# Kernel tuning notes

Measured on AMD Instinct MI355X. Metric: run time of the kernel, lower is better.

Reference implementation:

```python
import jax, jax.numpy as jnp
import numpy as np

FS = 11        # filter_size
N_ITER = 5     # mean-field iterations


def _unfold(x, fs):
    """x: (B, C, Hp, Wp) padded -> patches (B, C, H, W, fs, fs) with
    patches[b,c,h,w,i,j] == x[b,c,h+i,w+j]."""
    B, C, Hp, Wp = x.shape
    H, W = Hp - fs + 1, Wp - fs + 1
    p = jax.lax.conv_general_dilated_patches(
        x.reshape(B * C, 1, Hp, Wp), (fs, fs), (1, 1), 'VALID')  # (B*C, fs*fs, H, W)
    return p.reshape(B, C, fs, fs, H, W).transpose(0, 1, 4, 5, 2, 3)


def _smoothing_filter(fs, inv_bw, spacings):
    """Gaussian spatial filter with zeroed center, shape (B, fs, fs)."""
    r = jnp.arange(-(fs // 2), fs // 2 + 1, dtype=spacings.dtype)
    d = jnp.stack(jnp.meshgrid(r, r, indexing='ij'))           # (2, fs, fs)
    d = d[None] * spacings[:, :, None, None]                   # (B, 2, fs, fs)
    f = jnp.exp(-jnp.sum((d * inv_bw) ** 2 / 2, axis=1))       # (B, fs, fs)
    return f.at[:, fs // 2, fs // 2].set(0.0)


def setup_inputs() -> dict:
    key = jax.random.key(0)
    k1, k2 = jax.random.split(key)
    B, C, CH, H, W = 2, 6, 3, 192, 192
    return {
        'x': jax.random.normal(k1, (B, C, H, W), dtype=jnp.float32),
        'features': jax.random.normal(k2, (B, CH, H, W), dtype=jnp.float32),
        'spatial_spacings': jnp.ones((B, 2), dtype=jnp.float32),
        'smoothing_weight': jnp.array(1.0, dtype=jnp.float32),
        'appearance_weight': jnp.array(1.0, dtype=jnp.float32),
        'inverse_smoothing_bandwidth': jnp.array(1.0, dtype=jnp.float32),
        'inverse_appearance_bandwidth': jnp.array(1.0, dtype=jnp.float32),
    }


def reference(x, features, spatial_spacings, smoothing_weight, appearance_weight,
              inverse_smoothing_bandwidth, inverse_appearance_bandwidth):
    fs, pad = FS, FS // 2
    B, C, H, W = x.shape
    pad_cfg = [(0, 0), (0, 0), (pad, pad), (pad, pad)]

    # Spatial Gaussian filter (iteration-independent).
    sf = _smoothing_filter(fs, inverse_smoothing_bandwidth, spatial_spacings)  # (B,fs,fs)

    # Bilateral (appearance) filter, also iteration-independent -> hoisted.
    fpatch = _unfold(jnp.pad(features, pad_cfg), fs)           # (B,ch,H,W,fs,fs)
    diffs = features[..., None, None] - fpatch
    af = jnp.exp(-jnp.sum((diffs * inverse_appearance_bandwidth) ** 2 / 2, axis=1))  # (B,H,W,fs,fs)
    af = af.at[..., fs // 2, fs // 2].set(0.0)

    # combined message filter: w_s * sf + w_a * sf * af  (center tap already zero)
    sfb = sf[:, None, None]                                    # (B,1,1,fs,fs)
    total_filter = smoothing_weight * jnp.broadcast_to(sfb, af.shape) + appearance_weight * sfb * af

    compat = -jnp.eye(C, dtype=x.dtype)                        # Potts compatibility mu(l,l') = -[l==l']
    negative_unary = x
    for _ in range(N_ITER):
        q = jax.nn.softmax(x, axis=1)
        qpatch = _unfold(jnp.pad(q, pad_cfg), fs)              # (B,C,H,W,fs,fs)
        msg = jnp.einsum('bhwij,bchwij->bchw', total_filter, qpatch)
        x = negative_unary - jnp.einsum('bjhw,jk->bkhw', msg, compat)
    return jax.nn.log_softmax(x, axis=1)
```

## Files before the change

### kernel.cpp

```cpp
#include <hip/hip_runtime.h>

#define HH 192
#define WW 192
#define BB 2
#define NC 6
#define FSZ 11
#define PAD 5
#define TW 96
#define TH 3
#define SWD 107
#define SHT 14
#define LA 107
#define HW (HH*WW)
#define BT 768

__device__ __forceinline__ unsigned pkbf(float a, float b) {
    unsigned ua = (__float_as_uint(a) + 0x8000u) >> 16;
    unsigned ub = (__float_as_uint(b) + 0x8000u) & 0xffff0000u;
    return ua | ub;
}
__device__ __forceinline__ float lo16(unsigned u){ return __uint_as_float(u << 16); }
__device__ __forceinline__ float hi16(unsigned u){ return __uint_as_float(u & 0xffff0000u); }

template<bool FIRST, bool LAST>
__global__ __launch_bounds__(BT, 3)
void crf_it(const float* __restrict__ xpl, const uint4* __restrict__ Ain,
            const float* __restrict__ f2in, const float* __restrict__ feats,
            const float* __restrict__ spac, const float* __restrict__ swp,
            const float* __restrict__ awp, const float* __restrict__ isbp,
            const float* __restrict__ iabp,
            uint4* __restrict__ Aout, float* __restrict__ f2out,
            float* __restrict__ outp)
{
    __shared__ uint4 A[SHT][LA];
    __shared__ float F2[SHT][LA];
    __shared__ float sfw[FSZ*FSZ];
    __shared__ float sfa[FSZ*FSZ];

    const int tid = threadIdx.x;
    const int b  = blockIdx.z;
    const int w0 = blockIdx.x * TW;
    const int h0 = blockIdx.y * TH;

    const float sw  = swp[0], aw = awp[0], isb = isbp[0], iab = iabp[0];
    const float s0  = spac[b*2], s1 = spac[b*2+1];
    const float sfac = iab * 0.70710678f;

    if (tid < FSZ*FSZ) {
        const int fi = tid / FSZ, fj = tid - (tid/FSZ)*FSZ;
        const float ri = (float)(fi-PAD) * s0 * isb;
        const float rj = (float)(fj-PAD) * s1 * isb;
        float sf = __expf(-0.5f*(ri*ri + rj*rj));
        if (fi == PAD && fj == PAD) sf = 0.f;
        sfw[tid] = sf * sw;
        sfa[tid] = sf * aw;
    }

    for (int idx = tid; idx < SHT*SWD; idx += BT) {
        const int sr = idx / SWD, sc = idx - (idx/SWD)*SWD;
        const int gh = h0 + sr - PAD, gw = w0 + sc - PAD;
        uint4 av = make_uint4(0u,0u,0u,0u);
        float f2v = 0.f;
        if (gh >= 0 && gh < HH && gw >= 0 && gw < WW) {
            if (FIRST) {
                const int off = gh*WW + gw;
                const float* xb = xpl + (size_t)b*NC*HW + off;
                const float v0 = xb[0], v1 = xb[HW], v2 = xb[2*HW];
                const float v3 = xb[3*HW], v4 = xb[4*HW], v5 = xb[5*HW];
                float m = fmaxf(fmaxf(fmaxf(v0,v1),fmaxf(v2,v3)),fmaxf(v4,v5));
                float q0=__expf(v0-m), q1=__expf(v1-m), q2=__expf(v2-m);
                float q3=__expf(v3-m), q4=__expf(v4-m), q5=__expf(v5-m);
                const float rs = 1.0f/(q0+q1+q2+q3+q4+q5);
                const float* fb = feats + (size_t)b*3*HW + off;
                const float g0 = fb[0]*sfac, g1 = fb[HW]*sfac;
                f2v = fb[2*HW]*sfac;
                av = make_uint4(pkbf(q0*rs,q1*rs), pkbf(q2*rs,q3*rs),
                                pkbf(q4*rs,q5*rs), pkbf(g0,g1));
            } else {
                const size_t p = (size_t)(b*HH + gh)*WW + gw;
                av  = Ain[p];
                f2v = f2in[p];
            }
        }
        A[sr][sc]  = av;
        F2[sr][sc] = f2v;
    }
    __syncthreads();

    const int w    = tid >> 6;
    const int l    = tid & 63;
    const int t3   = l >> 3;
    const int rb   = (l >> 1) & 3;
    const int hf   = l & 1;
    const int prow = w >> 2;
    const int cb   = (w & 3)*24 + t3*3;
    const int jb   = hf*6;
    const int jcnt = hf ? 5 : 6;

    float cf0[3], cf1[3], cf2[3];
    #pragma unroll
    for (int k = 0; k < 3; ++k) {
        const uint4 cav = A[prow+PAD][cb+k+PAD];
        cf0[k] = lo16(cav.w);
        cf1[k] = hi16(cav.w);
        cf2[k] = F2[prow+PAD][cb+k+PAD];
    }

    float ms[3][NC];
    #pragma unroll
    for (int k = 0; k < 3; ++k)
        #pragma unroll
        for (int c = 0; c < NC; ++c) ms[k][c] = 0.f;

    #pragma unroll
    for (int m = 0; m < 3; ++m) {
        const int i = rb + 4*m;
        const bool vrow = (i < FSZ);
        float srwR[6], sraR[6];
        #pragma unroll
        for (int d = 0; d < 6; ++d) {
            const bool v = vrow && (d < jcnt);
            srwR[d] = v ? sfw[i*FSZ + jb + d] : 0.f;
            sraR[d] = v ? sfa[i*FSZ + jb + d] : 0.f;
        }
        const uint4* Ar = &A[prow + i][cb + jb];
        const float* Fr = &F2[prow + i][cb + jb];
        #pragma unroll
        for (int a = 0; a < 8; ++a) {
            const uint4 av = Ar[a];
            const float g2 = Fr[a];
            const float q0 = lo16(av.x), q1 = hi16(av.x);
            const float q2 = lo16(av.y), q3 = hi16(av.y);
            const float q4 = lo16(av.z), q5 = hi16(av.z);
            const float g0 = lo16(av.w), g1 = hi16(av.w);
            #pragma unroll
            for (int k = 0; k < 3; ++k) {
                const int d = a - k;
                if (0 <= d && d < 6) {
                    const float d0 = cf0[k]-g0, d1 = cf1[k]-g1, d2 = cf2[k]-g2;
                    const float t  = fmaf(d2,d2, fmaf(d1,d1, d0*d0));
                    const float af = __expf(-t);
                    const float tf = fmaf(af, sraR[d], srwR[d]);
                    ms[k][0] = fmaf(tf,q0,ms[k][0]);
                    ms[k][1] = fmaf(tf,q1,ms[k][1]);
                    ms[k][2] = fmaf(tf,q2,ms[k][2]);
                    ms[k][3] = fmaf(tf,q3,ms[k][3]);
                    ms[k][4] = fmaf(tf,q4,ms[k][4]);
                    ms[k][5] = fmaf(tf,q5,ms[k][5]);
                }
            }
        }
    }

    #pragma unroll
    for (int k = 0; k < 3; ++k)
        #pragma unroll
        for (int c = 0; c < NC; ++c) {
            float v = ms[k][c];
            v += __shfl_xor(v, 1);
            v += __shfl_xor(v, 2);
            v += __shfl_xor(v, 4);
            ms[k][c] = v;
        }

    if ((l & 7) == 0) {
        #pragma unroll
        for (int k = 0; k < 3; ++k) {
            const int oh = h0 + prow, ow = w0 + cb + k;
            const size_t pb = (size_t)b*NC*HW + (size_t)oh*WW + ow;
            float xn[NC];
            #pragma unroll
            for (int c = 0; c < NC; ++c) xn[c] = ms[k][c] + xpl[pb + (size_t)c*HW];

            float m = xn[0];
            #pragma unroll
            for (int c = 1; c < NC; ++c) m = fmaxf(m, xn[c]);

            if (LAST) {
                float s = 0.f;
                #pragma unroll
                for (int c = 0; c < NC; ++c) s += __expf(xn[c]-m);
                const float lg = m + __logf(s);
                #pragma unroll
                for (int c = 0; c < NC; ++c) outp[pb + (size_t)c*HW] = xn[c] - lg;
            } else {
                float e[NC], s = 0.f;
                #pragma unroll
                for (int c = 0; c < NC; ++c) { e[c] = __expf(xn[c]-m); s += e[c]; }
                const float rs = 1.0f / s;
                const size_t p = (size_t)(b*HH + oh)*WW + ow;
                Aout[p] = make_uint4(pkbf(e[0]*rs,e[1]*rs), pkbf(e[2]*rs,e[3]*rs),
                                     pkbf(e[4]*rs,e[5]*rs), pkbf(cf0[k],cf1[k]));
                if (FIRST) f2out[p] = cf2[k];
            }
        }
    }
}

extern "C" void kernel_launch(void* const* d_in, const int* in_sizes, int n_in,
                              void* d_out, int out_size, void* d_ws, size_t ws_size,
                              hipStream_t stream)
{
    const float* x    = (const float*)d_in[0];
    const float* fts  = (const float*)d_in[1];
    const float* spc  = (const float*)d_in[2];
    const float* swp  = (const float*)d_in[3];
    const float* awp  = (const float*)d_in[4];
    const float* isbp = (const float*)d_in[5];
    const float* iabp = (const float*)d_in[6];
    float* out = (float*)d_out;

    uint4* A0  = (uint4*)d_ws;
    uint4* A1  = A0 + (size_t)BB*HW;
    float* f2s = (float*)(A1 + (size_t)BB*HW);

    dim3 grid(WW/TW, HH/TH, BB);
    dim3 blk(BT);

    crf_it<true ,false><<<grid, blk, 0, stream>>>(x, A1, f2s, fts, spc, swp, awp, isbp, iabp, A0, f2s, out);
    crf_it<false,false><<<grid, blk, 0, stream>>>(x, A0, f2s, fts, spc, swp, awp, isbp, iabp, A1, f2s, out);
    crf_it<false,false><<<grid, blk, 0, stream>>>(x, A1, f2s, fts, spc, swp, awp, isbp, iabp, A0, f2s, out);
    crf_it<false,false><<<grid, blk, 0, stream>>>(x, A0, f2s, fts, spc, swp, awp, isbp, iabp, A1, f2s, out);
    crf_it<false,true ><<<grid, blk, 0, stream>>>(x, A1, f2s, fts, spc, swp, awp, isbp, iabp, A0, f2s, out);
}
```

Measured before the change: 65.69 us.

## Fuse pairs of mean-field iterations per kernel with halo recomputation

Replaces the five per-iteration launches with two fused kernels, each doing two mean-field iterations, plus a final kernel for the last iteration and the log-softmax. Each fused block loads a double-width halo, recomputes the intermediate softmax for its padded region in shared memory, then applies the second filter pass. Tiles change to 24x12, and the last stage splits the filter rows across two threads per pixel. This cuts launches and the global round trips of the intermediate state, but adds a lot of redundant halo compute (the first stage covers a 22x34 region for a 12x24 output tile) in an exp-heavy, compute-bound loop.

```diff
diff --git a/kernel.cpp b/kernel.cpp
--- a/kernel.cpp
+++ b/kernel.cpp
@@ -6,13 +6,19 @@
 #define NC 6
 #define FSZ 11
 #define PAD 5
-#define TW 96
-#define TH 3
-#define SWD 107
-#define SHT 14
-#define LA 107
+#define TW 24
+#define TH 12
 #define HW (HH*WW)
-#define BT 768
+
+#define S1R 32
+#define S1C 45
+#define Q1R 22
+#define Q1C 34
+#define BTA 768
+
+#define S3R 22
+#define S3C 35
+#define BTB 576
 
 __device__ __forceinline__ unsigned pkbf(float a, float b) {
     unsigned ua = (__float_as_uint(a) + 0x8000u) >> 16;
@@ -22,51 +28,56 @@
 __device__ __forceinline__ float lo16(unsigned u){ return __uint_as_float(u << 16); }
 __device__ __forceinline__ float hi16(unsigned u){ return __uint_as_float(u & 0xffff0000u); }
 
-template<bool FIRST, bool LAST>
-__global__ __launch_bounds__(BT, 3)
-void crf_it(const float* __restrict__ xpl, const uint4* __restrict__ Ain,
-            const float* __restrict__ f2in, const float* __restrict__ feats,
-            const float* __restrict__ spac, const float* __restrict__ swp,
-            const float* __restrict__ awp, const float* __restrict__ isbp,
-            const float* __restrict__ iabp,
-            uint4* __restrict__ Aout, float* __restrict__ f2out,
-            float* __restrict__ outp)
+__device__ __forceinline__ void build_sf(int tid, float s0, float s1, float isb,
+                                         float swv, float awv, float* sfw, float* sfa)
 {
-    __shared__ uint4 A[SHT][LA];
-    __shared__ float F2[SHT][LA];
-    __shared__ float sfw[FSZ*FSZ];
-    __shared__ float sfa[FSZ*FSZ];
+    if (tid < FSZ*FSZ) {
+        const int fi = tid / FSZ, fj = tid - (tid/FSZ)*FSZ;
+        const float ri = (float)(fi-PAD)*s0*isb;
+        const float rj = (float)(fj-PAD)*s1*isb;
+        float sf = __expf(-0.5f*(ri*ri+rj*rj));
+        if (fi==PAD && fj==PAD) sf = 0.f;
+        sfw[tid] = sf*swv;
+        sfa[tid] = sf*awv;
+    }
+}
+
+template<bool FIRST>
+__global__ __launch_bounds__(BTA, 3)
+void crf_duo(const float* __restrict__ xpl, const uint4* __restrict__ Ain,
+             const float* __restrict__ f2in, const float* __restrict__ feats,
+             const float* __restrict__ spac, const float* __restrict__ swp,
+             const float* __restrict__ awp, const float* __restrict__ isbp,
+             const float* __restrict__ iabp,
+             uint4* __restrict__ Aout, float* __restrict__ f2out)
+{
+    __shared__ uint4 A1[S1R][S1C];
+    __shared__ float F2a[S1R][S1C];
+    __shared__ uint4 Q1[Q1R][Q1C];
+    __shared__ float sfw[FSZ*FSZ], sfa[FSZ*FSZ];
 
     const int tid = threadIdx.x;
     const int b  = blockIdx.z;
     const int w0 = blockIdx.x * TW;
     const int h0 = blockIdx.y * TH;
 
-    const float sw  = swp[0], aw = awp[0], isb = isbp[0], iab = iabp[0];
-    const float s0  = spac[b*2], s1 = spac[b*2+1];
+    const float sw = swp[0], aw = awp[0], isb = isbp[0], iab = iabp[0];
+    const float s0 = spac[b*2], s1 = spac[b*2+1];
     const float sfac = iab * 0.70710678f;
 
-    if (tid < FSZ*FSZ) {
-        const int fi = tid / FSZ, fj = tid - (tid/FSZ)*FSZ;
-        const float ri = (float)(fi-PAD) * s0 * isb;
-        const float rj = (float)(fj-PAD) * s1 * isb;
-        float sf = __expf(-0.5f*(ri*ri + rj*rj));
-        if (fi == PAD && fj == PAD) sf = 0.f;
-        sfw[tid] = sf * sw;
-        sfa[tid] = sf * aw;
-    }
-
-    for (int idx = tid; idx < SHT*SWD; idx += BT) {
-        const int sr = idx / SWD, sc = idx - (idx/SWD)*SWD;
-        const int gh = h0 + sr - PAD, gw = w0 + sc - PAD;
+    build_sf(tid, s0, s1, isb, sw, aw, sfw, sfa);
+
+    for (int idx = tid; idx < S1R*S1C; idx += BTA) {
+        const int sr = idx / S1C, sc = idx - (idx/S1C)*S1C;
+        const int gh = h0 - 2*PAD + sr, gw = w0 - 2*PAD + sc;
         uint4 av = make_uint4(0u,0u,0u,0u);
         float f2v = 0.f;
         if (gh >= 0 && gh < HH && gw >= 0 && gw < WW) {
             if (FIRST) {
                 const int off = gh*WW + gw;
                 const float* xb = xpl + (size_t)b*NC*HW + off;
-                const float v0 = xb[0], v1 = xb[HW], v2 = xb[2*HW];
-                const float v3 = xb[3*HW], v4 = xb[4*HW], v5 = xb[5*HW];
+                const float v0=xb[0], v1=xb[HW], v2=xb[2*HW];
+                const float v3=xb[3*HW], v4=xb[4*HW], v5=xb[5*HW];
                 float m = fmaxf(fmaxf(fmaxf(v0,v1),fmaxf(v2,v3)),fmaxf(v4,v5));
                 float q0=__expf(v0-m), q1=__expf(v1-m), q2=__expf(v2-m);
                 float q3=__expf(v3-m), q4=__expf(v4-m), q5=__expf(v5-m);
@@ -82,117 +93,199 @@
                 f2v = f2in[p];
             }
         }
+        A1[sr][sc]  = av;
+        F2a[sr][sc] = f2v;
+    }
+    __syncthreads();
+
+    if (tid < Q1R*Q1C) {
+        const int pr = tid / Q1C, pc = tid - (tid/Q1C)*Q1C;
+        const int gh = h0 - PAD + pr, gw = w0 - PAD + pc;
+        uint4 qv = make_uint4(0u,0u,0u,0u);
+        if (gh >= 0 && gh < HH && gw >= 0 && gw < WW) {
+            const unsigned cw = A1[pr+PAD][pc+PAD].w;
+            const float cf0 = lo16(cw), cf1 = hi16(cw);
+            const float cf2 = F2a[pr+PAD][pc+PAD];
+            float msg[NC];
+            #pragma unroll
+            for (int c = 0; c < NC; ++c) msg[c] = 0.f;
+            #pragma unroll 1
+            for (int i = 0; i < FSZ; ++i) {
+                const float* srw = &sfw[i*FSZ];
+                const float* sra = &sfa[i*FSZ];
+                #pragma unroll
+                for (int j = 0; j < FSZ; ++j) {
+                    const uint4 av = A1[pr+i][pc+j];
+                    const float g2 = F2a[pr+i][pc+j];
+                    const float g0 = lo16(av.w), g1 = hi16(av.w);
+                    const float d0 = cf0-g0, d1 = cf1-g1, d2 = cf2-g2;
+                    const float t  = fmaf(d2,d2, fmaf(d1,d1, d0*d0));
+                    const float tf = fmaf(__expf(-t), sra[j], srw[j]);
+                    msg[0] = fmaf(tf, lo16(av.x), msg[0]);
+                    msg[1] = fmaf(tf, hi16(av.x), msg[1]);
+                    msg[2] = fmaf(tf, lo16(av.y), msg[2]);
+                    msg[3] = fmaf(tf, hi16(av.y), msg[3]);
+                    msg[4] = fmaf(tf, lo16(av.z), msg[4]);
+                    msg[5] = fmaf(tf, hi16(av.z), msg[5]);
+                }
+            }
+            const float* up = xpl + (size_t)b*NC*HW + (size_t)gh*WW + gw;
+            float xn[NC];
+            #pragma unroll
+            for (int c = 0; c < NC; ++c) xn[c] = msg[c] + up[(size_t)c*HW];
+            float m = xn[0];
+            #pragma unroll
+            for (int c = 1; c < NC; ++c) m = fmaxf(m, xn[c]);
+            float e[NC], s = 0.f;
+            #pragma unroll
+            for (int c = 0; c < NC; ++c) { e[c] = __expf(xn[c]-m); s += e[c]; }
+            const float rs = 1.0f / s;
+            qv = make_uint4(pkbf(e[0]*rs,e[1]*rs), pkbf(e[2]*rs,e[3]*rs),
+                            pkbf(e[4]*rs,e[5]*rs), 0u);
+        }
+        Q1[tid / Q1C][tid - (tid/Q1C)*Q1C] = qv;
+    }
+    __syncthreads();
+
+    if (tid < 2*TH*TW) {
+        const int p = tid >> 1, h = tid & 1;
+        const int qr = p / TW, qc = p - (p/TW)*TW;
+        const unsigned cw = A1[qr+2*PAD][qc+2*PAD].w;
+        const float cf0 = lo16(cw), cf1 = hi16(cw);
+        const float cf2 = F2a[qr+2*PAD][qc+2*PAD];
+        float msg[NC];
+        #pragma unroll
+        for (int c = 0; c < NC; ++c) msg[c] = 0.f;
+        const int i0 = h ? 6 : 0, i1 = h ? FSZ : 6;
+        #pragma unroll 1
+        for (int i = i0; i < i1; ++i) {
+            const float* srw = &sfw[i*FSZ];
+            const float* sra = &sfa[i*FSZ];
+            #pragma unroll
+            for (int j = 0; j < FSZ; ++j) {
+                const uint4 qv = Q1[qr+i][qc+j];
+                const uint4 fv = A1[qr+i+PAD][qc+j+PAD];
+                const float g2 = F2a[qr+i+PAD][qc+j+PAD];
+                const float g0 = lo16(fv.w), g1 = hi16(fv.w);
+                const float d0 = cf0-g0, d1 = cf1-g1, d2 = cf2-g2;
+                const float t  = fmaf(d2,d2, fmaf(d1,d1, d0*d0));
+                const float tf = fmaf(__expf(-t), sra[j], srw[j]);
+                msg[0] = fmaf(tf, lo16(qv.x), msg[0]);
+                msg[1] = fmaf(tf, hi16(qv.x), msg[1]);
+                msg[2] = fmaf(tf, lo16(qv.y), msg[2]);
+                msg[3] = fmaf(tf, hi16(qv.y), msg[3]);
+                msg[4] = fmaf(tf, lo16(qv.z), msg[4]);
+                msg[5] = fmaf(tf, hi16(qv.z), msg[5]);
+            }
+        }
+        #pragma unroll
+        for (int c = 0; c < NC; ++c) msg[c] += __shfl_xor(msg[c], 1);
+
+        if (h == 0) {
+            const int oh = h0 + qr, ow = w0 + qc;
+            const size_t pb = (size_t)b*NC*HW + (size_t)oh*WW + ow;
+            float xn[NC];
+            #pragma unroll
+            for (int c = 0; c < NC; ++c) xn[c] = msg[c] + xpl[pb + (size_t)c*HW];
+            float m = xn[0];
+            #pragma unroll
+            for (int c = 1; c < NC; ++c) m = fmaxf(m, xn[c]);
+            float e[NC], s = 0.f;
+            #pragma unroll
+            for (int c = 0; c < NC; ++c) { e[c] = __expf(xn[c]-m); s += e[c]; }
+            const float rs = 1.0f / s;
+            const size_t op = (size_t)(b*HH + oh)*WW + ow;
+            Aout[op] = make_uint4(pkbf(e[0]*rs,e[1]*rs), pkbf(e[2]*rs,e[3]*rs),
+                                  pkbf(e[4]*rs,e[5]*rs), cw);
+            if (FIRST) f2out[op] = cf2;
+        }
+    }
+}
+
+__global__ __launch_bounds__(BTB, 2)
+void crf_fin(const float* __restrict__ xpl, const uint4* __restrict__ Ain,
+             const float* __restrict__ f2in,
+             const float* __restrict__ spac, const float* __restrict__ swp,
+             const float* __restrict__ awp, const float* __restrict__ isbp,
+             const float* __restrict__ iabp, float* __restrict__ outp)
+{
+    __shared__ uint4 A[S3R][S3C];
+    __shared__ float F2[S3R][S3C];
+    __shared__ float sfw[FSZ*FSZ], sfa[FSZ*FSZ];
+
+    const int tid = threadIdx.x;
+    const int b  = blockIdx.z;
+    const int w0 = blockIdx.x * TW;
+    const int h0 = blockIdx.y * TH;
+
+    const float sw = swp[0], aw = awp[0], isb = isbp[0];
+    const float s0 = spac[b*2], s1 = spac[b*2+1];
+
+    build_sf(tid, s0, s1, isb, sw, aw, sfw, sfa);
+
+    for (int idx = tid; idx < S3R*S3C; idx += BTB) {
+        const int sr = idx / S3C, sc = idx - (idx/S3C)*S3C;
+        const int gh = h0 - PAD + sr, gw = w0 - PAD + sc;
+        uint4 av = make_uint4(0u,0u,0u,0u);
+        float f2v = 0.f;
+        if (gh >= 0 && gh < HH && gw >= 0 && gw < WW) {
+            const size_t p = (size_t)(b*HH + gh)*WW + gw;
+            av  = Ain[p];
+            f2v = f2in[p];
+        }
         A[sr][sc]  = av;
         F2[sr][sc] = f2v;
     }
     __syncthreads();
 
-    const int w    = tid >> 6;
-    const int l    = tid & 63;
-    const int t3   = l >> 3;
-    const int rb   = (l >> 1) & 3;
-    const int hf   = l & 1;
-    const int prow = w >> 2;
-    const int cb   = (w & 3)*24 + t3*3;
-    const int jb   = hf*6;
-    const int jcnt = hf ? 5 : 6;
-
-    float cf0[3], cf1[3], cf2[3];
-    #pragma unroll
-    for (int k = 0; k < 3; ++k) {
-        const uint4 cav = A[prow+PAD][cb+k+PAD];
-        cf0[k] = lo16(cav.w);
-        cf1[k] = hi16(cav.w);
-        cf2[k] = F2[prow+PAD][cb+k+PAD];
-    }
-
-    float ms[3][NC];
-    #pragma unroll
-    for (int k = 0; k < 3; ++k)
+    if (tid < 2*TH*TW) {
+        const int p = tid >> 1, h = tid & 1;
+        const int qr = p / TW, qc = p - (p/TW)*TW;
+        const unsigned cw = A[qr+PAD][qc+PAD].w;
+        const float cf0 = lo16(cw), cf1 = hi16(cw);
+        const float cf2 = F2[qr+PAD][qc+PAD];
+        float msg[NC];
         #pragma unroll
-        for (int c = 0; c < NC; ++c) ms[k][c] = 0.f;
-
-    #pragma unroll
-    for (int m = 0; m < 3; ++m) {
-        const int i = rb + 4*m;
-        const bool vrow = (i < FSZ);
-        float srwR[6], sraR[6];
+        for (int c = 0; c < NC; ++c) msg[c] = 0.f;
+        const int i0 = h ? 6 : 0, i1 = h ? FSZ : 6;
+        #pragma unroll 1
+        for (int i = i0; i < i1; ++i) {
+            const float* srw = &sfw[i*FSZ];
+            const float* sra = &sfa[i*FSZ];
+            #pragma unroll
+            for (int j = 0; j < FSZ; ++j) {
+                const uint4 qv = A[qr+i][qc+j];
+                const float g2 = F2[qr+i][qc+j];
+                const float g0 = lo16(qv.w), g1 = hi16(qv.w);
+                const float d0 = cf0-g0, d1 = cf1-g1, d2 = cf2-g2;
+                const float t  = fmaf(d2,d2, fmaf(d1,d1, d0*d0));
+                const float tf = fmaf(__expf(-t), sra[j], srw[j]);
+                msg[0] = fmaf(tf, lo16(qv.x), msg[0]);
+                msg[1] = fmaf(tf, hi16(qv.x), msg[1]);
+                msg[2] = fmaf(tf, lo16(qv.y), msg[2]);
+                msg[3] = fmaf(tf, hi16(qv.y), msg[3]);
+                msg[4] = fmaf(tf, lo16(qv.z), msg[4]);
+                msg[5] = fmaf(tf, hi16(qv.z), msg[5]);
+            }
+        }
         #pragma unroll
-        for (int d = 0; d < 6; ++d) {
-            const bool v = vrow && (d < jcnt);
-            srwR[d] = v ? sfw[i*FSZ + jb + d] : 0.f;
-            sraR[d] = v ? sfa[i*FSZ + jb + d] : 0.f;
-        }
-        const uint4* Ar = &A[prow + i][cb + jb];
-        const float* Fr = &F2[prow + i][cb + jb];
-        #pragma unroll
-        for (int a = 0; a < 8; ++a) {
-            const uint4 av = Ar[a];
-            const float g2 = Fr[a];
-            const float q0 = lo16(av.x), q1 = hi16(av.x);
-            const float q2 = lo16(av.y), q3 = hi16(av.y);
-            const float q4 = lo16(av.z), q5 = hi16(av.z);
-            const float g0 = lo16(av.w), g1 = hi16(av.w);
-            #pragma unroll
-            for (int k = 0; k < 3; ++k) {
-                const int d = a - k;
-                if (0 <= d && d < 6) {
-                    const float d0 = cf0[k]-g0, d1 = cf1[k]-g1, d2 = cf2[k]-g2;
-                    const float t  = fmaf(d2,d2, fmaf(d1,d1, d0*d0));
-                    const float af = __expf(-t);
-                    const float tf = fmaf(af, sraR[d], srwR[d]);
-                    ms[k][0] = fmaf(tf,q0,ms[k][0]);
-                    ms[k][1] = fmaf(tf,q1,ms[k][1]);
-                    ms[k][2] = fmaf(tf,q2,ms[k][2]);
-                    ms[k][3] = fmaf(tf,q3,ms[k][3]);
-                    ms[k][4] = fmaf(tf,q4,ms[k][4]);
-                    ms[k][5] = fmaf(tf,q5,ms[k][5]);
-                }
-            }
-        }
-    }
-
-    #pragma unroll
-    for (int k = 0; k < 3; ++k)
-        #pragma unroll
-        for (int c = 0; c < NC; ++c) {
-            float v = ms[k][c];
-            v += __shfl_xor(v, 1);
-            v += __shfl_xor(v, 2);
-            v += __shfl_xor(v, 4);
-            ms[k][c] = v;
-        }
-
-    if ((l & 7) == 0) {
-        #pragma unroll
-        for (int k = 0; k < 3; ++k) {
-            const int oh = h0 + prow, ow = w0 + cb + k;
+        for (int c = 0; c < NC; ++c) msg[c] += __shfl_xor(msg[c], 1);
+
+        if (h == 0) {
+            const int oh = h0 + qr, ow = w0 + qc;
             const size_t pb = (size_t)b*NC*HW + (size_t)oh*WW + ow;
             float xn[NC];
             #pragma unroll
-            for (int c = 0; c < NC; ++c) xn[c] = ms[k][c] + xpl[pb + (size_t)c*HW];
-
+            for (int c = 0; c < NC; ++c) xn[c] = msg[c] + xpl[pb + (size_t)c*HW];
             float m = xn[0];
             #pragma unroll
             for (int c = 1; c < NC; ++c) m = fmaxf(m, xn[c]);
-
-            if (LAST) {
-                float s = 0.f;
-                #pragma unroll
-                for (int c = 0; c < NC; ++c) s += __expf(xn[c]-m);
-                const float lg = m + __logf(s);
-                #pragma unroll
-                for (int c = 0; c < NC; ++c) outp[pb + (size_t)c*HW] = xn[c] - lg;
-            } else {
-                float e[NC], s = 0.f;
-                #pragma unroll
-                for (int c = 0; c < NC; ++c) { e[c] = __expf(xn[c]-m); s += e[c]; }
-                const float rs = 1.0f / s;
-                const size_t p = (size_t)(b*HH + oh)*WW + ow;
-                Aout[p] = make_uint4(pkbf(e[0]*rs,e[1]*rs), pkbf(e[2]*rs,e[3]*rs),
-                                     pkbf(e[4]*rs,e[5]*rs), pkbf(cf0[k],cf1[k]));
-                if (FIRST) f2out[p] = cf2[k];
-            }
+            float s = 0.f;
+            #pragma unroll
+            for (int c = 0; c < NC; ++c) s += __expf(xn[c]-m);
+            const float lg = m + __logf(s);
+            #pragma unroll
+            for (int c = 0; c < NC; ++c) outp[pb + (size_t)c*HW] = xn[c] - lg;
         }
     }
 }
@@ -210,16 +303,13 @@
     const float* iabp = (const float*)d_in[6];
     float* out = (float*)d_out;
 
-    uint4* A0  = (uint4*)d_ws;
-    uint4* A1  = A0 + (size_t)BB*HW;
-    float* f2s = (float*)(A1 + (size_t)BB*HW);
+    uint4* S0  = (uint4*)d_ws;
+    uint4* S1  = S0 + (size_t)BB*HW;
+    float* f2s = (float*)(S1 + (size_t)BB*HW);
 
     dim3 grid(WW/TW, HH/TH, BB);
-    dim3 blk(BT);
-
-    crf_it<true ,false><<<grid, blk, 0, stream>>>(x, A1, f2s, fts, spc, swp, awp, isbp, iabp, A0, f2s, out);
-    crf_it<false,false><<<grid, blk, 0, stream>>>(x, A0, f2s, fts, spc, swp, awp, isbp, iabp, A1, f2s, out);
-    crf_it<false,false><<<grid, blk, 0, stream>>>(x, A1, f2s, fts, spc, swp, awp, isbp, iabp, A0, f2s, out);
-    crf_it<false,false><<<grid, blk, 0, stream>>>(x, A0, f2s, fts, spc, swp, awp, isbp, iabp, A1, f2s, out);
-    crf_it<false,true ><<<grid, blk, 0, stream>>>(x, A1, f2s, fts, spc, swp, awp, isbp, iabp, A0, f2s, out);
-}
+
+    crf_duo<true ><<<grid, dim3(BTA), 0, stream>>>(x, S1, f2s, fts, spc, swp, awp, isbp, iabp, S0, f2s);
+    crf_duo<false><<<grid, dim3(BTA), 0, stream>>>(x, S0, f2s, fts, spc, swp, awp, isbp, iabp, S1, f2s);
+    crf_fin<<<grid, dim3(BTB), 0, stream>>>(x, S1, f2s, spc, swp, awp, isbp, iabp, out);
+}
```

Result: slower. 71.81 us (+9.3%).
